# Kernel tuning notes

Hardware: AMD Instinct MI355X
Metric: run time of the kernel (lower is better)

The kernel has to match this reference:

```python
import math
import jax, jax.numpy as jnp
import numpy as np

B, N, D = 4, 4096, 1024
H, DH = 16, 64  # D == H * DH


def setup_inputs() -> dict:
    key = jax.random.key(0)
    ks = jax.random.split(key, 7)
    s = 1.0 / math.sqrt(D)
    return {
        "tens": jax.random.normal(ks[0], (B, N, D), dtype=jnp.float32),
        "Wq": jax.random.normal(ks[1], (D, D), dtype=jnp.float32) * s,
        "bq": jax.random.normal(ks[2], (D,), dtype=jnp.float32) * 0.01,
        "Wk": jax.random.normal(ks[3], (D, D), dtype=jnp.float32) * s,
        "bk": jax.random.normal(ks[4], (D,), dtype=jnp.float32) * 0.01,
        "Wv": jax.random.normal(ks[5], (D, D), dtype=jnp.float32) * s,
        "bv": jax.random.normal(ks[6], (D,), dtype=jnp.float32) * 0.01,
    }


def reference(tens, Wq, bq, Wk, bk, Wv, bv):
    b, n, d = tens.shape
    # projections (torch Linear: x @ W^T + b)
    q = (tens @ Wq.T + bq).reshape(b, n, H, DH)  # [B,N,H,DH]
    k = (tens @ Wk.T + bk).reshape(b, n, H, DH)
    v = (tens @ Wv.T + bv).reshape(b, n, H, DH)
    scale = (1.0 / math.sqrt(DH)) / math.sqrt(n)
    # No softmax between QK^T and V => linear, reassociate as Q @ (K^T V)
    # to avoid the O(N^2) attention matrix; identical math.
    ktv = jnp.einsum("bnhd,bnhe->bhde", k, v)          # [B,H,DH,DH]
    out = jnp.einsum("bnhd,bhde->bnhe", q, ktv) * scale  # [B,N,H,DH]
    return out.reshape(b, n, d)
```

## Files before the change

### kernel.cpp

```cpp
#include <hip/hip_runtime.h>

typedef unsigned short ushort_t;
typedef __attribute__((ext_vector_type(8))) __bf16 bf16x8;
typedef __attribute__((ext_vector_type(8))) unsigned short ushort8;
typedef __attribute__((ext_vector_type(4))) unsigned short ushort4_t;
typedef __attribute__((ext_vector_type(4))) float floatx4;

__device__ inline unsigned short f2bf(float f) {
  union { float f; unsigned u; } x; x.f = f;
  return (unsigned short)((x.u + 0x7FFFu + ((x.u >> 16) & 1u)) >> 16);
}
__device__ inline float bf2f(unsigned short v) {
  union { unsigned u; float f; } x; x.u = (unsigned)v << 16;
  return x.f;
}

__global__ void cvt_tr(const float* __restrict__ tens, ushort_t* __restrict__ Xbf,
                       ushort_t* __restrict__ XT, float* __restrict__ spart,
                       const float* __restrict__ Wk, ushort_t* __restrict__ Wkbf,
                       const float* __restrict__ Wv, ushort_t* __restrict__ Wvbf) {
  int t = threadIdx.x;
  if (blockIdx.z == 4) {
    int flat = blockIdx.x + 16 * blockIdx.y;
    const float* in; ushort_t* out;
    if (flat < 512) { in = Wk; out = Wkbf; } else { in = Wv; out = Wvbf; flat -= 512; }
    int i = (flat * 256 + t) * 8;
    const float4* p = (const float4*)(in + i);
    float4 x = p[0], y = p[1];
    ushort8 o;
    o[0] = f2bf(x.x); o[1] = f2bf(x.y); o[2] = f2bf(x.z); o[3] = f2bf(x.w);
    o[4] = f2bf(y.x); o[5] = f2bf(y.y); o[6] = f2bf(y.z); o[7] = f2bf(y.w);
    *(ushort8*)(out + i) = o;
    return;
  }
  int b = blockIdx.z;
  int d0 = blockIdx.x * 64;
  int n0 = blockIdx.y * 64;
  __shared__ ushort_t sT[64 * 72];
  int nl = t >> 2, c16 = (t & 3) * 16;
  const float* src = tens + ((long)b << 22) + (long)(n0 + nl) * 1024 + d0 + c16;
  ushort8 o0, o1;
#pragma unroll
  for (int j = 0; j < 2; ++j) {
    float4 v0 = *(const float4*)(src + j * 8);
    float4 v1 = *(const float4*)(src + j * 8 + 4);
    ushort8 o;
    o[0] = f2bf(v0.x); o[1] = f2bf(v0.y); o[2] = f2bf(v0.z); o[3] = f2bf(v0.w);
    o[4] = f2bf(v1.x); o[5] = f2bf(v1.y); o[6] = f2bf(v1.z); o[7] = f2bf(v1.w);
#pragma unroll
    for (int i = 0; i < 8; ++i) sT[(c16 + j * 8 + i) * 72 + nl] = o[i];
    if (j == 0) o0 = o; else o1 = o;
  }
  ushort_t* xdst = Xbf + ((long)b << 22) + (long)(n0 + nl) * 1024 + d0 + c16;
  *(ushort8*)xdst = o0;
  *(ushort8*)(xdst + 8) = o1;
  __syncthreads();
  int dl = t >> 2, n16 = (t & 3) * 16;
  ushort8 t0 = *(const ushort8*)(sT + dl * 72 + n16);
  ushort8 t1 = *(const ushort8*)(sT + dl * 72 + n16 + 8);
  ushort_t* dst = XT + ((long)b << 22) + (long)(d0 + dl) * 4096 + n0 + n16;
  *(ushort8*)dst = t0;
  *(ushort8*)(dst + 8) = t1;
  float ps = 0.f;
#pragma unroll
  for (int i = 0; i < 8; ++i) ps += bf2f(t0[i]) + bf2f(t1[i]);
  ps += __shfl_xor(ps, 1);
  ps += __shfl_xor(ps, 2);
  if ((t & 3) == 0) spart[(((long)b << 6) + blockIdx.y) * 1024 + d0 + dl] = ps;
}

__device__ inline void gload_lds16(const void* g, void* l) {
  __builtin_amdgcn_global_load_lds(
      (const __attribute__((address_space(1))) unsigned int*)g,
      (__attribute__((address_space(3))) unsigned int*)l, 16, 0, 0);
}

template <int K>
__global__ void gemm_bt(const ushort_t* __restrict__ A, const ushort_t* __restrict__ Bm,
                        const float* __restrict__ bias, float* __restrict__ C,
                        int N, long sA_, long sB_, long sBias_, long sC_) {
  int gx = gridDim.x, gxy = gridDim.x * gridDim.y;
  int flat = blockIdx.x + gx * blockIdx.y + gxy * blockIdx.z;
  int total = gxy * gridDim.z;
  int per = total >> 3;
  int nf = (flat & 7) * per + (flat >> 3);
  int bz = nf / gxy; int rem = nf - bz * gxy;
  int by = rem / gx; int bx = rem - by * gx;

  A += (long)bz * sA_; Bm += (long)bz * sB_; C += (long)bz * sC_;
  bias += (long)bz * sBias_;

  __shared__ ushort_t sA[2][128 * 32];
  __shared__ ushort_t sB[2][128 * 32];

  int t = threadIdx.x;
  int w = t >> 6, l = t & 63;
  int wy = w >> 1, wx = w & 1;
  int quad = l >> 4, m16 = l & 15;
  int mBase = by * 128, nBase = bx * 128;

  int r = l >> 2, pk = l & 3;
  int sCol = (pk ^ ((r >> 1) & 3)) * 8;
  int sRow0 = w * 32 + r;
  const ushort_t* gA0 = A + (long)(mBase + sRow0) * K + sCol;
  const ushort_t* gA1 = gA0 + 16 * K;
  const ushort_t* gB0 = Bm + (long)(nBase + sRow0) * K + sCol;
  const ushort_t* gB1 = gB0 + 16 * K;
  int lOff0 = (w * 2) * 512;
  int lOff1 = lOff0 + 512;

  int swzR = (m16 >> 1) & 3;
  int aOff = (wy * 64 + m16) * 32 + (quad ^ swzR) * 8;
  int bOff = (wx * 64 + m16) * 32 + (quad ^ swzR) * 8;

  floatx4 acc[4][4] = {};
  const int NS = K / 32;

  gload_lds16(gA0, sA[0] + lOff0);
  gload_lds16(gA1, sA[0] + lOff1);
  gload_lds16(gB0, sB[0] + lOff0);
  gload_lds16(gB1, sB[0] + lOff1);
  __syncthreads();

  for (int kt = 0; kt < NS; ++kt) {
    if (kt + 1 < NS) {
      int nb = (kt + 1) & 1, ko = (kt + 1) * 32;
      gload_lds16(gA0 + ko, sA[nb] + lOff0);
      gload_lds16(gA1 + ko, sA[nb] + lOff1);
      gload_lds16(gB0 + ko, sB[nb] + lOff0);
      gload_lds16(gB1 + ko, sB[nb] + lOff1);
    }
    __builtin_amdgcn_sched_barrier(0);
    const ushort_t* pa = sA[kt & 1];
    const ushort_t* pbm = sB[kt & 1];
    bf16x8 af[4], bfr[4];
#pragma unroll
    for (int i = 0; i < 4; ++i) af[i] = *(const bf16x8*)(pa + aOff + i * 16 * 32);
#pragma unroll
    for (int i = 0; i < 4; ++i) bfr[i] = *(const bf16x8*)(pbm + bOff + i * 16 * 32);
#pragma unroll
    for (int mi = 0; mi < 4; ++mi)
#pragma unroll
      for (int ni = 0; ni < 4; ++ni)
        acc[mi][ni] = __builtin_amdgcn_mfma_f32_16x16x32_bf16(bfr[ni], af[mi], acc[mi][ni], 0, 0, 0);
    if (kt + 1 < NS) __syncthreads();
  }

#pragma unroll
  for (int mi = 0; mi < 4; ++mi) {
    int m = mBase + wy * 64 + mi * 16 + m16;
    float* crow = C + (long)m * N;
#pragma unroll
    for (int ni = 0; ni < 4; ++ni) {
      int n0 = nBase + wx * 64 + ni * 16 + quad * 4;
      float4 bb = *(const float4*)(bias + n0);
      floatx4 v = acc[mi][ni];
      float4 o;
      o.x = v[0] + bb.x; o.y = v[1] + bb.y; o.z = v[2] + bb.z; o.w = v[3] + bb.w;
      *(float4*)(crow + n0) = o;
    }
  }
}

template <int K, bool SYM, bool UW>
__global__ void gemm64(const ushort_t* __restrict__ A, const ushort_t* __restrict__ Bm,
                       ushort_t* __restrict__ C, int N, long sA_, long sB_, long sC_,
                       const ushort_t* __restrict__ Wkbf, const ushort_t* __restrict__ Wvbf,
                       const float* __restrict__ spart, float* __restrict__ u,
                       float* __restrict__ wv_s) {
  __shared__ ushort_t sA[2][2][64 * 32];
  __shared__ ushort_t sB[2][2][64 * 32];
  int t = threadIdx.x;

  int bz, byy, bxx;
  if (SYM) {
    int flat = blockIdx.x + gridDim.x * blockIdx.y;
    int per = (gridDim.x * gridDim.y) >> 3;
    int nf = (flat & 7) * per + (flat >> 3);
    if (UW) {
      if (nf >= 544) {
        int id = nf - 544;
        int b = id & 3, which = (id >> 2) & 1, chunk = id >> 3;
        const ushort_t* W = which ? Wvbf : Wkbf;
        float* o = which ? wv_s : u;
        float* ss = (float*)sA;
        float4 a4 = {0.f, 0.f, 0.f, 0.f};
        const float* sp = spart + ((long)b << 16) + t * 4;
        for (int n0 = 0; n0 < 64; ++n0) {
          float4 v = *(const float4*)(sp + n0 * 1024);
          a4.x += v.x; a4.y += v.y; a4.z += v.z; a4.w += v.w;
        }
        *(float4*)(ss + t * 4) = a4;
        __syncthreads();
        int rr = chunk * 256 + t;
        const ushort_t* row = W + (long)rr * 1024;
        float acc = 0.f;
        for (int k = 0; k < 1024; k += 8) {
          ushort8 v = *(const ushort8*)(row + k);
#pragma unroll
          for (int i = 0; i < 8; ++i) acc += bf2f(v[i]) * ss[k + i];
        }
        o[b * 1024 + rr] = acc;
        return;
      }
    }
    bz = nf / 136;
    int tri = nf - bz * 136;
    byy = (int)((__fsqrt_rn(8.0f * tri + 1.0f) - 1.0f) * 0.5f);
    while ((byy + 1) * (byy + 2) / 2 <= tri) ++byy;
    while (byy * (byy + 1) / 2 > tri) --byy;
    bxx = tri - byy * (byy + 1) / 2;
  } else {
    int gx = gridDim.x, gxy = gridDim.x * gridDim.y;
    int flat = blockIdx.x + gx * blockIdx.y + gxy * blockIdx.z;
    int total = gxy * gridDim.z;
    int per = total >> 3;
    int nf = (flat & 7) * per + (flat >> 3);
    bz = nf / gxy; int rem = nf - bz * gxy;
    byy = rem / gx; bxx = rem - byy * gx;
  }

  A += (long)bz * sA_; Bm += (long)bz * sB_; C += (long)bz * sC_;

  int w = t >> 6, l = t & 63;
  int wy = w >> 1, wx = w & 1;
  int quad = l >> 4, m16 = l & 15;
  int mBase = byy * 64, nBase = bxx * 64;

  int r = l >> 2, pk = l & 3;
  int sCol = (pk ^ ((r >> 1) & 3)) * 8;
  int sRow = w * 16 + r;
  const ushort_t* gA = A + (long)(mBase + sRow) * K + sCol;
  const ushort_t* gB = Bm + (long)(nBase + sRow) * K + sCol;
  int lOff = w * 512;

  int swzR = (m16 >> 1) & 3;
  int aOff = (wy * 32 + m16) * 32 + (quad ^ swzR) * 8;
  int bOff = (wx * 32 + m16) * 32 + (quad ^ swzR) * 8;

  floatx4 acc[2][2] = {};
  const int NS = K / 64;

#pragma unroll
  for (int kk = 0; kk < 2; ++kk) {
    gload_lds16(gA + kk * 32, sA[0][kk] + lOff);
    gload_lds16(gB + kk * 32, sB[0][kk] + lOff);
  }
  __syncthreads();

  for (int kt = 0; kt < NS; ++kt) {
    if (kt + 1 < NS) {
      int nb = (kt + 1) & 1, ko = (kt + 1) * 64;
#pragma unroll
      for (int kk = 0; kk < 2; ++kk) {
        gload_lds16(gA + ko + kk * 32, sA[nb][kk] + lOff);
        gload_lds16(gB + ko + kk * 32, sB[nb][kk] + lOff);
      }
    }
    __builtin_amdgcn_sched_barrier(0);
    int cb = kt & 1;
#pragma unroll
    for (int kk = 0; kk < 2; ++kk) {
      bf16x8 af0 = *(const bf16x8*)(sA[cb][kk] + aOff);
      bf16x8 af1 = *(const bf16x8*)(sA[cb][kk] + aOff + 16 * 32);
      bf16x8 bf0 = *(const bf16x8*)(sB[cb][kk] + bOff);
      bf16x8 bf1 = *(const bf16x8*)(sB[cb][kk] + bOff + 16 * 32);
      acc[0][0] = __builtin_amdgcn_mfma_f32_16x16x32_bf16(af0, bf0, acc[0][0], 0, 0, 0);
      acc[0][1] = __builtin_amdgcn_mfma_f32_16x16x32_bf16(af0, bf1, acc[0][1], 0, 0, 0);
      acc[1][0] = __builtin_amdgcn_mfma_f32_16x16x32_bf16(af1, bf0, acc[1][0], 0, 0, 0);
      acc[1][1] = __builtin_amdgcn_mfma_f32_16x16x32_bf16(af1, bf1, acc[1][1], 0, 0, 0);
    }
    if (kt + 1 < NS) __syncthreads();
  }

#pragma unroll
  for (int ni = 0; ni < 2; ++ni) {
    int n = nBase + wx * 32 + ni * 16 + m16;
#pragma unroll
    for (int mi = 0; mi < 2; ++mi) {
      int m0 = mBase + wy * 32 + mi * 16 + quad * 4;
      floatx4 v = acc[mi][ni];
#pragma unroll
      for (int rr = 0; rr < 4; ++rr)
        C[(long)(m0 + rr) * N + n] = f2bf(v[rr]);
      if (SYM) {
        if (byy != bxx) {
          ushort4_t pkv;
#pragma unroll
          for (int rr = 0; rr < 4; ++rr) pkv[rr] = f2bf(v[rr]);
          *(ushort4_t*)(C + (long)n * N + m0) = pkv;
        }
      }
    }
  }
}

__global__ void ktv_small(const ushort_t* __restrict__ T1, const ushort_t* __restrict__ Wvbf,
                          const float* __restrict__ u, const float* __restrict__ wv_s,
                          const float* __restrict__ bk, const float* __restrict__ bv,
                          float* __restrict__ ktv) {
  int bh = blockIdx.x; int b = bh >> 4, h = bh & 15;
  int t = threadIdx.x, w = t >> 6, l = t & 63;
  int quad = l >> 4, m16 = l & 15;
  const ushort_t* Arow = T1 + ((long)b << 20) + (long)(h * 64 + w * 16 + m16) * 1024 + quad * 8;
  const ushort_t* Brow = Wvbf + (long)(h * 64 + m16) * 1024 + quad * 8;
  floatx4 acc[4] = {};
  for (int kt = 0; kt < 1024; kt += 32) {
    bf16x8 af = *(const bf16x8*)(Arow + kt);
#pragma unroll
    for (int j = 0; j < 4; ++j) {
      bf16x8 bfv = *(const bf16x8*)(Brow + (long)j * 16 * 1024 + kt);
      acc[j] = __builtin_amdgcn_mfma_f32_16x16x32_bf16(af, bfv, acc[j], 0, 0, 0);
    }
  }
  float* p = ktv + (long)bh * 4096;
#pragma unroll
  for (int j = 0; j < 4; ++j) {
    int e = j * 16 + m16;
    float bve = bv[h * 64 + e];
    float wse = wv_s[b * 1024 + h * 64 + e] + 4096.f * bve;
#pragma unroll
    for (int rr = 0; rr < 4; ++rr) {
      int d = w * 16 + quad * 4 + rr;
      float corr = u[b * 1024 + h * 64 + d] * bve + bk[h * 64 + d] * wse;
      p[d * 64 + e] = acc[j][rr] + corr;
    }
  }
}

__global__ void make_w2(const float* __restrict__ Wq, const float* __restrict__ bq,
                        const float* __restrict__ ktv, ushort_t* __restrict__ W2T,
                        float* __restrict__ bias2, float scale) {
  int bh = blockIdx.x, cq = blockIdx.y;
  int b = bh >> 4, h = bh & 15;
  __shared__ float sKTV[64 * 64];
  __shared__ float sW[64 * 64];
  int t = threadIdx.x;
  for (int i = t * 4; i < 4096; i += 1024)
    *(float4*)(sKTV + i) = *(const float4*)(ktv + (long)bh * 4096 + i);
  __syncthreads();
  if (cq == 0 && t < 64) {
    float s = 0.f;
    for (int d = 0; d < 64; ++d) s += bq[h * 64 + d] * sKTV[d * 64 + t];
    bias2[b * 1024 + h * 64 + t] = s * scale;
  }
  int e = t >> 2, c0 = (t & 3) * 16;
  for (int ct = cq * 256; ct < cq * 256 + 256; ct += 64) {
    __syncthreads();
    {
      int d = t >> 2, cc = (t & 3) * 16;
#pragma unroll
      for (int j = 0; j < 16; j += 4)
        *(float4*)(sW + d * 64 + cc + j) =
            *(const float4*)(Wq + (long)(h * 64 + d) * 1024 + ct + cc + j);
    }
    __syncthreads();
    float outv[16] = {};
    for (int d = 0; d < 64; ++d) {
      float kv = sKTV[d * 64 + e];
#pragma unroll
      for (int j = 0; j < 16; ++j) outv[j] += sW[d * 64 + c0 + j] * kv;
    }
    ushort8 o0, o1;
#pragma unroll
    for (int j = 0; j < 8; ++j) { o0[j] = f2bf(outv[j] * scale); o1[j] = f2bf(outv[8 + j] * scale); }
    ushort_t* dst = W2T + ((long)(b * 1024 + h * 64 + e)) * 1024 + ct + c0;
    *(ushort8*)dst = o0;
    *(ushort8*)(dst + 8) = o1;
  }
}

extern "C" void kernel_launch(void* const* d_in, const int* in_sizes, int n_in,
                              void* d_out, int out_size, void* d_ws, size_t ws_size,
                              hipStream_t stream) {
  (void)in_sizes; (void)n_in; (void)out_size; (void)ws_size;
  const float* tens = (const float*)d_in[0];
  const float* Wq = (const float*)d_in[1];
  const float* bq = (const float*)d_in[2];
  const float* Wk = (const float*)d_in[3];
  const float* bk = (const float*)d_in[4];
  const float* Wv = (const float*)d_in[5];
  const float* bv = (const float*)d_in[6];
  float* out = (float*)d_out;

  char* w = (char*)d_ws;
  ushort_t* Xbf  = (ushort_t*)(w);
  ushort_t* XT   = (ushort_t*)(w + 33554432);
  ushort_t* Wkbf = (ushort_t*)(w + 67108864);
  ushort_t* Wvbf = (ushort_t*)(w + 69206016);
  ushort_t* Gbf  = (ushort_t*)(w + 71303168);
  ushort_t* T1   = (ushort_t*)(w + 79691776);
  float*    spart= (float*)(w + 88080384);
  float*    u    = (float*)(w + 89128960);
  float*    wv_s = (float*)(w + 89145344);
  float*    ktv  = (float*)(w + 89161728);
  ushort_t* W2T  = (ushort_t*)(w + 90210304);
  float*    bias2= (float*)(w + 98598912);

  const float scale = (1.0f / 8.0f) / 64.0f;

  hipLaunchKernelGGL(cvt_tr, dim3(16, 64, 5), dim3(256), 0, stream,
                     tens, Xbf, XT, spart, Wk, Wkbf, Wv, Wvbf);

  hipLaunchKernelGGL((gemm64<4096, true, true>), dim3(144, 4, 1), dim3(256), 0, stream,
                     XT, XT, Gbf, 1024, 4194304L, 4194304L, 1048576L,
                     Wkbf, Wvbf, spart, u, wv_s);

  hipLaunchKernelGGL((gemm64<1024, false, false>), dim3(16, 16, 4), dim3(256), 0, stream,
                     Wkbf, Gbf, T1, 1024, 0L, 1048576L, 1048576L,
                     (const ushort_t*)nullptr, (const ushort_t*)nullptr,
                     (const float*)nullptr, (float*)nullptr, (float*)nullptr);

  hipLaunchKernelGGL(ktv_small, dim3(64), dim3(256), 0, stream,
                     T1, Wvbf, u, wv_s, bk, bv, ktv);

  hipLaunchKernelGGL(make_w2, dim3(64, 4), dim3(256), 0, stream,
                     Wq, bq, ktv, W2T, bias2, scale);

  hipLaunchKernelGGL((gemm_bt<1024>), dim3(8, 32, 4), dim3(256), 0, stream,
                     Xbf, W2T, bias2, out, 1024,
                     4194304L, 1048576L, 1024L, 4194304L);
}
```

Baseline: 289.4 us.

## Replace final projection GEMM with 256x256-tile 512-thread kernel using K=64 stages

```diff
diff --git a/kernel.cpp b/kernel.cpp
--- a/kernel.cpp
+++ b/kernel.cpp
@@ -14,6 +14,13 @@
   union { unsigned u; float f; } x; x.u = (unsigned)v << 16;
   return x.f;
 }
+
+__device__ inline void bar() {
+  asm volatile("" ::: "memory");
+  __builtin_amdgcn_s_barrier();
+  asm volatile("" ::: "memory");
+}
+#define WAITV0 asm volatile("s_waitcnt vmcnt(0)" ::: "memory")
 
 __global__ void cvt_tr(const float* __restrict__ tens, ushort_t* __restrict__ Xbf,
                        ushort_t* __restrict__ XT, float* __restrict__ spart,
@@ -76,9 +83,11 @@
 }
 
 template <int K>
-__global__ void gemm_bt(const ushort_t* __restrict__ A, const ushort_t* __restrict__ Bm,
-                        const float* __restrict__ bias, float* __restrict__ C,
-                        int N, long sA_, long sB_, long sBias_, long sC_) {
+__global__ __launch_bounds__(512, 2) void gemm256(
+    const ushort_t* __restrict__ A, const ushort_t* __restrict__ Bm,
+    const float* __restrict__ bias, float* __restrict__ C,
+    int N, long sA_, long sB_, long sBias_, long sC_) {
+  const int NT = K / 64;
   int gx = gridDim.x, gxy = gridDim.x * gridDim.y;
   int flat = blockIdx.x + gx * blockIdx.y + gxy * blockIdx.z;
   int total = gxy * gridDim.z;
@@ -90,74 +99,92 @@
   A += (long)bz * sA_; Bm += (long)bz * sB_; C += (long)bz * sC_;
   bias += (long)bz * sBias_;
 
-  __shared__ ushort_t sA[2][128 * 32];
-  __shared__ ushort_t sB[2][128 * 32];
+  __shared__ ushort_t sA[2][16384];
+  __shared__ ushort_t sB[2][16384];
 
   int t = threadIdx.x;
   int w = t >> 6, l = t & 63;
-  int wy = w >> 1, wx = w & 1;
+  int wy = w >> 2, wx = w & 3;
   int quad = l >> 4, m16 = l & 15;
-  int mBase = by * 128, nBase = bx * 128;
-
-  int r = l >> 2, pk = l & 3;
-  int sCol = (pk ^ ((r >> 1) & 3)) * 8;
-  int sRow0 = w * 32 + r;
-  const ushort_t* gA0 = A + (long)(mBase + sRow0) * K + sCol;
-  const ushort_t* gA1 = gA0 + 16 * K;
-  const ushort_t* gB0 = Bm + (long)(nBase + sRow0) * K + sCol;
-  const ushort_t* gB1 = gB0 + 16 * K;
-  int lOff0 = (w * 2) * 512;
-  int lOff1 = lOff0 + 512;
-
-  int swzR = (m16 >> 1) & 3;
-  int aOff = (wy * 64 + m16) * 32 + (quad ^ swzR) * 8;
-  int bOff = (wx * 64 + m16) * 32 + (quad ^ swzR) * 8;
-
-  floatx4 acc[4][4] = {};
-  const int NS = K / 32;
-
-  gload_lds16(gA0, sA[0] + lOff0);
-  gload_lds16(gA1, sA[0] + lOff1);
-  gload_lds16(gB0, sB[0] + lOff0);
-  gload_lds16(gB1, sB[0] + lOff1);
-  __syncthreads();
-
-  for (int kt = 0; kt < NS; ++kt) {
-    if (kt + 1 < NS) {
-      int nb = (kt + 1) & 1, ko = (kt + 1) * 32;
-      gload_lds16(gA0 + ko, sA[nb] + lOff0);
-      gload_lds16(gA1 + ko, sA[nb] + lOff1);
-      gload_lds16(gB0 + ko, sB[nb] + lOff0);
-      gload_lds16(gB1 + ko, sB[nb] + lOff1);
-    }
-    __builtin_amdgcn_sched_barrier(0);
-    const ushort_t* pa = sA[kt & 1];
-    const ushort_t* pbm = sB[kt & 1];
-    bf16x8 af[4], bfr[4];
-#pragma unroll
-    for (int i = 0; i < 4; ++i) af[i] = *(const bf16x8*)(pa + aOff + i * 16 * 32);
-#pragma unroll
-    for (int i = 0; i < 4; ++i) bfr[i] = *(const bf16x8*)(pbm + bOff + i * 16 * 32);
-#pragma unroll
-    for (int mi = 0; mi < 4; ++mi)
-#pragma unroll
-      for (int ni = 0; ni < 4; ++ni)
-        acc[mi][ni] = __builtin_amdgcn_mfma_f32_16x16x32_bf16(bfr[ni], af[mi], acc[mi][ni], 0, 0, 0);
-    if (kt + 1 < NS) __syncthreads();
-  }
-
-#pragma unroll
-  for (int mi = 0; mi < 4; ++mi) {
-    int m = mBase + wy * 64 + mi * 16 + m16;
-    float* crow = C + (long)m * N;
-#pragma unroll
-    for (int ni = 0; ni < 4; ++ni) {
-      int n0 = nBase + wx * 64 + ni * 16 + quad * 4;
-      float4 bb = *(const float4*)(bias + n0);
+  int mBase = by * 256, nBase = bx * 256;
+
+  int rp = w * 8 + (l >> 3);
+  int ce = (((l & 7) * 16) ^ (((l >> 5) & 1) << 5)) >> 1;
+  const ushort_t* gAp[4]; const ushort_t* gBp[4];
+#pragma unroll
+  for (int h = 0; h < 2; ++h)
+#pragma unroll
+    for (int g = 0; g < 2; ++g) {
+      gAp[h * 2 + g] = A + (long)(mBase + h * 128 + g * 64 + rp) * K + ce;
+      gBp[h * 2 + g] = Bm + (long)(nBase + h * 128 + g * 64 + rp) * K + ce;
+    }
+
+  int swzu = ((m16 >> 2) & 1) << 4;
+  int aBase = wy * 8192 + m16 * 64;
+  int bBase = (wx >> 1) * 8192 + ((wx & 1) * 64 + m16) * 64;
+
+  floatx4 acc[8][4] = {};
+
+  auto STAGE = [&](int kt, int buf) {
+    int ko = kt * 64;
+#pragma unroll
+    for (int g = 0; g < 2; ++g) {
+      gload_lds16(gAp[g] + ko,     sA[buf] + g * 4096 + w * 512);
+      gload_lds16(gAp[2 + g] + ko, sA[buf] + 8192 + g * 4096 + w * 512);
+      gload_lds16(gBp[g] + ko,     sB[buf] + g * 4096 + w * 512);
+      gload_lds16(gBp[2 + g] + ko, sB[buf] + 8192 + g * 4096 + w * 512);
+    }
+  };
+
+#define PHASE(buf, mg, ks, LOADB)                                            \
+  {                                                                          \
+    const ushort_t* pa = sA[buf];                                            \
+    const ushort_t* pb = sB[buf];                                            \
+    if (LOADB) {                                                             \
+      _Pragma("unroll") for (int ni = 0; ni < 4; ++ni)                       \
+          bfr[ni] = *(const bf16x8*)(pb + bBase + ni * 16 * 64 +             \
+                                     (((ks) * 32 + quad * 8) ^ swzu));       \
+    }                                                                        \
+    bf16x8 af[4];                                                            \
+    _Pragma("unroll") for (int i = 0; i < 4; ++i)                            \
+        af[i] = *(const bf16x8*)(pa + aBase + ((mg) * 4 + i) * 16 * 64 +     \
+                                 (((ks) * 32 + quad * 8) ^ swzu));           \
+    __builtin_amdgcn_s_setprio(1);                                           \
+    _Pragma("unroll") for (int i = 0; i < 4; ++i)                            \
+        _Pragma("unroll") for (int ni = 0; ni < 4; ++ni)                     \
+            acc[(mg) * 4 + i][ni] = __builtin_amdgcn_mfma_f32_16x16x32_bf16( \
+                af[i], bfr[ni], acc[(mg) * 4 + i][ni], 0, 0, 0);             \
+    __builtin_amdgcn_s_setprio(0);                                           \
+    bar();                                                                   \
+  }
+
+  STAGE(0, 0);
+  WAITV0;
+  bar();
+  for (int kt = 0; kt < NT; ++kt) {
+    int buf = kt & 1;
+    if (kt + 1 < NT) STAGE(kt + 1, buf ^ 1);
+    bf16x8 bfr[4];
+    PHASE(buf, 0, 0, true);
+    PHASE(buf, 1, 0, false);
+    PHASE(buf, 0, 1, true);
+    PHASE(buf, 1, 1, false);
+    if (kt + 1 < NT) { WAITV0; }
+    bar();
+  }
+#undef PHASE
+
+#pragma unroll
+  for (int ni = 0; ni < 4; ++ni) {
+    int n = nBase + wx * 64 + ni * 16 + m16;
+    float bb = bias[n];
+#pragma unroll
+    for (int mi = 0; mi < 8; ++mi) {
+      int m0 = mBase + wy * 128 + mi * 16 + quad * 4;
       floatx4 v = acc[mi][ni];
-      float4 o;
-      o.x = v[0] + bb.x; o.y = v[1] + bb.y; o.z = v[2] + bb.z; o.w = v[3] + bb.w;
-      *(float4*)(crow + n0) = o;
+#pragma unroll
+      for (int rr = 0; rr < 4; ++rr)
+        C[(long)(m0 + rr) * N + n] = v[rr] + bb;
     }
   }
 }
@@ -417,7 +444,7 @@
   hipLaunchKernelGGL(make_w2, dim3(64, 4), dim3(256), 0, stream,
                      Wq, bq, ktv, W2T, bias2, scale);
 
-  hipLaunchKernelGGL((gemm_bt<1024>), dim3(8, 32, 4), dim3(256), 0, stream,
+  hipLaunchKernelGGL((gemm256<1024>), dim3(4, 16, 4), dim3(512), 0, stream,
                      Xbf, W2T, bias2, out, 1024,
                      4194304L, 1048576L, 1024L, 4194304L);
 }
```

Result: slower. 296.8 us (+2.5%).

## Split-K the Gram matrix GEMM into two halves with a separate reduce kernel

Applied to the files above, without the earlier changes.

```diff
diff --git a/kernel.cpp b/kernel.cpp
--- a/kernel.cpp
+++ b/kernel.cpp
@@ -3,7 +3,6 @@
 typedef unsigned short ushort_t;
 typedef __attribute__((ext_vector_type(8))) __bf16 bf16x8;
 typedef __attribute__((ext_vector_type(8))) unsigned short ushort8;
-typedef __attribute__((ext_vector_type(4))) unsigned short ushort4_t;
 typedef __attribute__((ext_vector_type(4))) float floatx4;
 
 __device__ inline unsigned short f2bf(float f) {
@@ -162,65 +161,49 @@
   }
 }
 
-template <int K, bool SYM, bool UW>
-__global__ void gemm64(const ushort_t* __restrict__ A, const ushort_t* __restrict__ Bm,
-                       ushort_t* __restrict__ C, int N, long sA_, long sB_, long sC_,
+__global__ void gsplit(const ushort_t* __restrict__ XT, float* __restrict__ part,
                        const ushort_t* __restrict__ Wkbf, const ushort_t* __restrict__ Wvbf,
                        const float* __restrict__ spart, float* __restrict__ u,
                        float* __restrict__ wv_s) {
   __shared__ ushort_t sA[2][2][64 * 32];
   __shared__ ushort_t sB[2][2][64 * 32];
   int t = threadIdx.x;
-
-  int bz, byy, bxx;
-  if (SYM) {
-    int flat = blockIdx.x + gridDim.x * blockIdx.y;
-    int per = (gridDim.x * gridDim.y) >> 3;
-    int nf = (flat & 7) * per + (flat >> 3);
-    if (UW) {
-      if (nf >= 544) {
-        int id = nf - 544;
-        int b = id & 3, which = (id >> 2) & 1, chunk = id >> 3;
-        const ushort_t* W = which ? Wvbf : Wkbf;
-        float* o = which ? wv_s : u;
-        float* ss = (float*)sA;
-        float4 a4 = {0.f, 0.f, 0.f, 0.f};
-        const float* sp = spart + ((long)b << 16) + t * 4;
-        for (int n0 = 0; n0 < 64; ++n0) {
-          float4 v = *(const float4*)(sp + n0 * 1024);
-          a4.x += v.x; a4.y += v.y; a4.z += v.z; a4.w += v.w;
-        }
-        *(float4*)(ss + t * 4) = a4;
-        __syncthreads();
-        int rr = chunk * 256 + t;
-        const ushort_t* row = W + (long)rr * 1024;
-        float acc = 0.f;
-        for (int k = 0; k < 1024; k += 8) {
-          ushort8 v = *(const ushort8*)(row + k);
-#pragma unroll
-          for (int i = 0; i < 8; ++i) acc += bf2f(v[i]) * ss[k + i];
-        }
-        o[b * 1024 + rr] = acc;
-        return;
-      }
-    }
-    bz = nf / 136;
-    int tri = nf - bz * 136;
-    byy = (int)((__fsqrt_rn(8.0f * tri + 1.0f) - 1.0f) * 0.5f);
-    while ((byy + 1) * (byy + 2) / 2 <= tri) ++byy;
-    while (byy * (byy + 1) / 2 > tri) --byy;
-    bxx = tri - byy * (byy + 1) / 2;
-  } else {
-    int gx = gridDim.x, gxy = gridDim.x * gridDim.y;
-    int flat = blockIdx.x + gx * blockIdx.y + gxy * blockIdx.z;
-    int total = gxy * gridDim.z;
-    int per = total >> 3;
-    int nf = (flat & 7) * per + (flat >> 3);
-    bz = nf / gxy; int rem = nf - bz * gxy;
-    byy = rem / gx; bxx = rem - byy * gx;
-  }
-
-  A += (long)bz * sA_; Bm += (long)bz * sB_; C += (long)bz * sC_;
+  int flat = blockIdx.x + 140 * blockIdx.y;
+  int nf = (flat & 7) * 140 + (flat >> 3);
+  if (nf >= 1088) {
+    int id = nf - 1088;
+    int b = id & 3, which = (id >> 2) & 1, chunk = id >> 3;
+    const ushort_t* W = which ? Wvbf : Wkbf;
+    float* o = which ? wv_s : u;
+    float* ss = (float*)sA;
+    float4 a4 = {0.f, 0.f, 0.f, 0.f};
+    const float* sp = spart + ((long)b << 16) + t * 4;
+    for (int n0 = 0; n0 < 64; ++n0) {
+      float4 v = *(const float4*)(sp + n0 * 1024);
+      a4.x += v.x; a4.y += v.y; a4.z += v.z; a4.w += v.w;
+    }
+    *(float4*)(ss + t * 4) = a4;
+    __syncthreads();
+    int rr = chunk * 256 + t;
+    const ushort_t* row = W + (long)rr * 1024;
+    float acc = 0.f;
+    for (int k = 0; k < 1024; k += 8) {
+      ushort8 v = *(const ushort8*)(row + k);
+#pragma unroll
+      for (int i = 0; i < 8; ++i) acc += bf2f(v[i]) * ss[k + i];
+    }
+    o[b * 1024 + rr] = acc;
+    return;
+  }
+  int bz = nf / 136;
+  int tri = nf - bz * 136;
+  int b = bz & 3, half = bz >> 2;
+  int byy = (int)((__fsqrt_rn(8.0f * tri + 1.0f) - 1.0f) * 0.5f);
+  while ((byy + 1) * (byy + 2) / 2 <= tri) ++byy;
+  while (byy * (byy + 1) / 2 > tri) --byy;
+  int bxx = tri - byy * (byy + 1) / 2;
+
+  const ushort_t* Abase = XT + ((long)b << 22) + half * 2048;
 
   int w = t >> 6, l = t & 63;
   int wy = w >> 1, wx = w & 1;
@@ -230,8 +213,8 @@
   int r = l >> 2, pk = l & 3;
   int sCol = (pk ^ ((r >> 1) & 3)) * 8;
   int sRow = w * 16 + r;
-  const ushort_t* gA = A + (long)(mBase + sRow) * K + sCol;
-  const ushort_t* gB = Bm + (long)(nBase + sRow) * K + sCol;
+  const ushort_t* gA = Abase + (long)(mBase + sRow) * 4096 + sCol;
+  const ushort_t* gB = Abase + (long)(nBase + sRow) * 4096 + sCol;
   int lOff = w * 512;
 
   int swzR = (m16 >> 1) & 3;
@@ -239,7 +222,7 @@
   int bOff = (wx * 32 + m16) * 32 + (quad ^ swzR) * 8;
 
   floatx4 acc[2][2] = {};
-  const int NS = K / 64;
+  const int NS = 32;
 
 #pragma unroll
   for (int kk = 0; kk < 2; ++kk) {
@@ -273,6 +256,119 @@
     if (kt + 1 < NS) __syncthreads();
   }
 
+  float* pt = part + ((long)(bz * 136 + tri)) * 4096;
+#pragma unroll
+  for (int ni = 0; ni < 2; ++ni) {
+    int n = wx * 32 + ni * 16 + m16;
+#pragma unroll
+    for (int mi = 0; mi < 2; ++mi) {
+      int m0 = wy * 32 + mi * 16 + quad * 4;
+      floatx4 v = acc[mi][ni];
+#pragma unroll
+      for (int rr = 0; rr < 4; ++rr) pt[(m0 + rr) * 64 + n] = v[rr];
+    }
+  }
+}
+
+__global__ void greduce(const float* __restrict__ part, ushort_t* __restrict__ Gbf) {
+  int tri = blockIdx.x, b = blockIdx.y;
+  int byy = (int)((__fsqrt_rn(8.0f * tri + 1.0f) - 1.0f) * 0.5f);
+  while ((byy + 1) * (byy + 2) / 2 <= tri) ++byy;
+  while (byy * (byy + 1) / 2 > tri) --byy;
+  int bxx = tri - byy * (byy + 1) / 2;
+  int t = threadIdx.x;
+  int r = t >> 2, c0 = (t & 3) * 16;
+  const float* p0 = part + ((long)(b * 136 + tri)) * 4096 + r * 64 + c0;
+  const float* p1 = p0 + (long)544 * 4096;
+  ushort_t vv[16];
+#pragma unroll
+  for (int j = 0; j < 16; j += 4) {
+    float4 a = *(const float4*)(p0 + j);
+    float4 bb = *(const float4*)(p1 + j);
+    vv[j + 0] = f2bf(a.x + bb.x); vv[j + 1] = f2bf(a.y + bb.y);
+    vv[j + 2] = f2bf(a.z + bb.z); vv[j + 3] = f2bf(a.w + bb.w);
+  }
+  ushort_t* g = Gbf + ((long)b << 20);
+  ushort_t* drow = g + (long)(byy * 64 + r) * 1024 + bxx * 64 + c0;
+  ushort8 o0, o1;
+#pragma unroll
+  for (int j = 0; j < 8; ++j) { o0[j] = vv[j]; o1[j] = vv[8 + j]; }
+  *(ushort8*)drow = o0;
+  *(ushort8*)(drow + 8) = o1;
+  if (byy != bxx) {
+#pragma unroll
+    for (int j = 0; j < 16; ++j)
+      g[(long)(bxx * 64 + c0 + j) * 1024 + byy * 64 + r] = vv[j];
+  }
+}
+
+template <int K>
+__global__ void gemm64(const ushort_t* __restrict__ A, const ushort_t* __restrict__ Bm,
+                       ushort_t* __restrict__ C, int N, long sA_, long sB_, long sC_) {
+  __shared__ ushort_t sA[2][2][64 * 32];
+  __shared__ ushort_t sB[2][2][64 * 32];
+  int t = threadIdx.x;
+  int gx = gridDim.x, gxy = gridDim.x * gridDim.y;
+  int flat = blockIdx.x + gx * blockIdx.y + gxy * blockIdx.z;
+  int total = gxy * gridDim.z;
+  int per = total >> 3;
+  int nf = (flat & 7) * per + (flat >> 3);
+  int bz = nf / gxy; int rem = nf - bz * gxy;
+  int byy = rem / gx; int bxx = rem - byy * gx;
+
+  A += (long)bz * sA_; Bm += (long)bz * sB_; C += (long)bz * sC_;
+
+  int w = t >> 6, l = t & 63;
+  int wy = w >> 1, wx = w & 1;
+  int quad = l >> 4, m16 = l & 15;
+  int mBase = byy * 64, nBase = bxx * 64;
+
+  int r = l >> 2, pk = l & 3;
+  int sCol = (pk ^ ((r >> 1) & 3)) * 8;
+  int sRow = w * 16 + r;
+  const ushort_t* gA = A + (long)(mBase + sRow) * K + sCol;
+  const ushort_t* gB = Bm + (long)(nBase + sRow) * K + sCol;
+  int lOff = w * 512;
+
+  int swzR = (m16 >> 1) & 3;
+  int aOff = (wy * 32 + m16) * 32 + (quad ^ swzR) * 8;
+  int bOff = (wx * 32 + m16) * 32 + (quad ^ swzR) * 8;
+
+  floatx4 acc[2][2] = {};
+  const int NS = K / 64;
+
+#pragma unroll
+  for (int kk = 0; kk < 2; ++kk) {
+    gload_lds16(gA + kk * 32, sA[0][kk] + lOff);
+    gload_lds16(gB + kk * 32, sB[0][kk] + lOff);
+  }
+  __syncthreads();
+
+  for (int kt = 0; kt < NS; ++kt) {
+    if (kt + 1 < NS) {
+      int nb = (kt + 1) & 1, ko = (kt + 1) * 64;
+#pragma unroll
+      for (int kk = 0; kk < 2; ++kk) {
+        gload_lds16(gA + ko + kk * 32, sA[nb][kk] + lOff);
+        gload_lds16(gB + ko + kk * 32, sB[nb][kk] + lOff);
+      }
+    }
+    __builtin_amdgcn_sched_barrier(0);
+    int cb = kt & 1;
+#pragma unroll
+    for (int kk = 0; kk < 2; ++kk) {
+      bf16x8 af0 = *(const bf16x8*)(sA[cb][kk] + aOff);
+      bf16x8 af1 = *(const bf16x8*)(sA[cb][kk] + aOff + 16 * 32);
+      bf16x8 bf0 = *(const bf16x8*)(sB[cb][kk] + bOff);
+      bf16x8 bf1 = *(const bf16x8*)(sB[cb][kk] + bOff + 16 * 32);
+      acc[0][0] = __builtin_amdgcn_mfma_f32_16x16x32_bf16(af0, bf0, acc[0][0], 0, 0, 0);
+      acc[0][1] = __builtin_amdgcn_mfma_f32_16x16x32_bf16(af0, bf1, acc[0][1], 0, 0, 0);
+      acc[1][0] = __builtin_amdgcn_mfma_f32_16x16x32_bf16(af1, bf0, acc[1][0], 0, 0, 0);
+      acc[1][1] = __builtin_amdgcn_mfma_f32_16x16x32_bf16(af1, bf1, acc[1][1], 0, 0, 0);
+    }
+    if (kt + 1 < NS) __syncthreads();
+  }
+
 #pragma unroll
   for (int ni = 0; ni < 2; ++ni) {
     int n = nBase + wx * 32 + ni * 16 + m16;
@@ -283,14 +379,6 @@
 #pragma unroll
       for (int rr = 0; rr < 4; ++rr)
         C[(long)(m0 + rr) * N + n] = f2bf(v[rr]);
-      if (SYM) {
-        if (byy != bxx) {
-          ushort4_t pkv;
-#pragma unroll
-          for (int rr = 0; rr < 4; ++rr) pkv[rr] = f2bf(v[rr]);
-          *(ushort4_t*)(C + (long)n * N + m0) = pkv;
-        }
-      }
     }
   }
 }
@@ -396,20 +484,19 @@
   float*    ktv  = (float*)(w + 89161728);
   ushort_t* W2T  = (ushort_t*)(w + 90210304);
   float*    bias2= (float*)(w + 98598912);
+  float*    part = (float*)(w + 98615296);
 
   const float scale = (1.0f / 8.0f) / 64.0f;
 
   hipLaunchKernelGGL(cvt_tr, dim3(16, 64, 5), dim3(256), 0, stream,
                      tens, Xbf, XT, spart, Wk, Wkbf, Wv, Wvbf);
 
-  hipLaunchKernelGGL((gemm64<4096, true, true>), dim3(144, 4, 1), dim3(256), 0, stream,
-                     XT, XT, Gbf, 1024, 4194304L, 4194304L, 1048576L,
-                     Wkbf, Wvbf, spart, u, wv_s);
-
-  hipLaunchKernelGGL((gemm64<1024, false, false>), dim3(16, 16, 4), dim3(256), 0, stream,
-                     Wkbf, Gbf, T1, 1024, 0L, 1048576L, 1048576L,
-                     (const ushort_t*)nullptr, (const ushort_t*)nullptr,
-                     (const float*)nullptr, (float*)nullptr, (float*)nullptr);
+  hipLaunchKernelGGL(gsplit, dim3(140, 8), dim3(256), 0, stream,
+                     XT, part, Wkbf, Wvbf, spart, u, wv_s);
+  hipLaunchKernelGGL(greduce, dim3(136, 4), dim3(256), 0, stream, part, Gbf);
+
+  hipLaunchKernelGGL((gemm64<1024>), dim3(16, 16, 4), dim3(256), 0, stream,
+                     Wkbf, Gbf, T1, 1024, 0L, 1048576L, 1048576L);
 
   hipLaunchKernelGGL(ktv_small, dim3(64), dim3(256), 0, stream,
                      T1, Wvbf, u, wv_s, bk, bv, ktv);
```

Measured after the change: 314.3 us. +8.6%, slower.
